# Optimization experiments

Hardware: AMD Instinct MI355X
Metric: run time of the kernel (lower is better)

Reference implementation:

```python
import jax, jax.numpy as jnp
import numpy as np

SAMPLERATE = 22050
N_OCTAVES = 16
N_SAMPLES = 32768
MIN_FREQ = 20.0 / (SAMPLERATE // 2)
MAX_FREQ = 3000.0 / (SAMPLERATE // 2)
FREQ_RANGE = MAX_FREQ - MIN_FREQ
BASE_RESONANCE = 0.01


def max_norm(x, axis=-1, eps=1e-8):
    return x / (jnp.max(jnp.abs(x), axis=axis, keepdims=True) + eps)


def exponential_decay(decay_values, n_octaves):
    # decay_values: (B, E, 1). Note the original applies sigmoid here on top of
    # the sigmoid already applied in forward (sigmoid_decay=True) -> double sigmoid.
    dv = jax.nn.sigmoid(decay_values)  # (B, E, 1)
    resonance_factor = (1.0 - BASE_RESONANCE) * 0.99
    decay = BASE_RESONANCE + dv * resonance_factor  # (B, E, 1)
    logd = jnp.log(decay + 1e-12)
    b, e, _ = decay_values.shape
    # cumsum of a per-(b,e) constant over octaves, then exp (matches torch code;
    # F.interpolate to size==n_octaves is the identity here)
    logd = jnp.broadcast_to(logd, (b, e, n_octaves))
    return jnp.exp(jnp.cumsum(logd, axis=-1))  # (B, E, O)


def setup_inputs() -> dict:
    key = jax.random.key(0)
    k1, k2, k3 = jax.random.split(key, 3)
    B, E = 8, 64
    return {
        "f0": jax.random.uniform(k1, (B, E, 1), dtype=jnp.float32),
        "decay_coefficients": jax.random.normal(k2, (B, E, 1), dtype=jnp.float32),
        "unused": jnp.zeros((B, E, 1), dtype=jnp.float32),
        "freq_spacing": jax.random.uniform(k3, (B, E, 1), dtype=jnp.float32),
    }


def reference(f0, decay_coefficients, unused, freq_spacing):
    b, e, _ = f0.shape
    O, S = N_OCTAVES, N_SAMPLES

    f0 = jnp.abs(f0)  # (B, E, 1)
    # sigmoid_decay=True path: sigmoid applied before exponential_decay
    exp_decays = exponential_decay(jax.nn.sigmoid(decay_coefficients), O)  # (B, E, O)

    f0 = (MIN_FREQ + f0 * FREQ_RANGE) * jnp.pi  # (B, E, 1)

    # freq_spacing repeated over octaves then cumsum -> per-octave factors
    factors = jnp.cumsum(jnp.broadcast_to(freq_spacing, (b, e, O)), axis=-1)
    f0s = f0 * factors  # (B, E, O)

    # nyquist cutoff
    f0s = f0s * (f0s < 1.0)

    # phase: cumsum over samples of constant per-octave frequency (faithful to torch)
    phase = jnp.cumsum(jnp.broadcast_to(f0s[..., None], (b, e, O, S)), axis=-1)
    osc = jnp.sin(phase)  # (B, E, O, S)

    osc = osc * exp_decays[..., None]
    osc = jnp.sum(osc, axis=2)  # (B, E, S)
    return max_norm(osc, axis=-1)
```

## Files before the change

### kernel.cpp

```cpp
#include <hip/hip_runtime.h>
#include <hip/hip_fp16.h>
#include <math.h>

#define N_OCT 16
#define NPAIR 8
#define NS    32768
#define TPB   512
#define SPT   (NS / TPB)
#define N_BE  512

typedef float v2f __attribute__((ext_vector_type(2)));
typedef _Float16 h4 __attribute__((ext_vector_type(4)));

static __device__ __forceinline__ v2f fma2(v2f a, v2f b, v2f c) {
    return __builtin_elementwise_fma(a, b, c);
}

#define WS_R(ws)    ((double*)(ws))
#define WS_C2H(ws)  ((float*)((char*)(ws) + 65536))
#define WS_C2L(ws)  ((float*)((char*)(ws) + 98304))
#define WS_AMP(ws)  ((float*)((char*)(ws) + 131072))

__global__ __launch_bounds__(256)
void f0res_setup(const float* __restrict__ f0_in,
                 const float* __restrict__ dc_in,
                 const float* __restrict__ fs_in,
                 void* __restrict__ ws)
{
    const int idx = blockIdx.x * 256 + threadIdx.x;
    if (idx >= N_BE * N_OCT) return;
    const int be = idx >> 4, o = idx & 15;

    const float f0a = fabsf(f0_in[be]);
    const float dc  = dc_in[be];
    const float fs  = fs_in[be];

    const float MINF = (float)(20.0 / 11025.0);
    const float FRNG = (float)(3000.0 / 11025.0 - 20.0 / 11025.0);

    const float s1    = 1.0f / (1.0f + __expf(-dc));
    const float dv    = 1.0f / (1.0f + __expf(-s1));
    const float decay = 0.01f + dv * 0.9801f;
    const float logd  = __logf(decay + 1e-12f);
    const float f0r   = (MINF + f0a * FRNG) * 3.14159274101257324f;

    float cl = 0.f, cf = 0.f;
    for (int i = 0; i <= o; ++i) { cl += logd; cf += fs; }
    float ed  = __expf(cl);
    float f0s = f0r * cf;
    float a   = ed;
    if (!(f0s < 1.0f)) { a = 0.0f; f0s = 0.0f; }

    const double inv2pi = 0.15915494309189535;
    double r = (double)f0s * inv2pi;

    double drev = r * (double)TPB;
    drev -= floor(drev);
    double c2d = 2.0 * cos(drev * 6.283185307179586);
    float  ch  = (float)c2d;

    WS_R(ws)[idx]   = r;
    WS_C2H(ws)[idx] = ch;
    WS_C2L(ws)[idx] = (float)(c2d - (double)ch);
    WS_AMP(ws)[idx] = a;
}

__global__ __launch_bounds__(TPB, 1)
void f0res_kernel(const void* __restrict__ ws,
                  float* __restrict__ out)
{
    extern __shared__ _Float16 smem[];
    __shared__ float wmax[TPB / 64];

    const int be = blockIdx.x;
    const int t  = threadIdx.x;

    const double* __restrict__ Rtab = WS_R(ws)   + be * N_OCT;
    const float*  __restrict__ CH   = WS_C2H(ws) + be * N_OCT;
    const float*  __restrict__ CLo  = WS_C2L(ws) + be * N_OCT;
    const float*  __restrict__ AMP  = WS_AMP(ws) + be * N_OCT;

    v2f xp[NPAIR], xc[NPAIR], c2h[NPAIR], c2l[NPAIR];

    #pragma unroll
    for (int o = 0; o < N_OCT; ++o) {
        const double r = Rtab[o];
        const float  a = AMP[o];

        double p0 = r * (double)(t + 1);
        p0 -= floor(p0);
        double pm = r * (double)(t + 1 - TPB);
        pm -= floor(pm);
        float xcur  = a * __builtin_amdgcn_sinf((float)p0);
        float xprev = a * __builtin_amdgcn_sinf((float)pm);

        const int j = o >> 1;
        if ((o & 1) == 0) {
            xc[j].x = xcur;   xp[j].x = xprev;
            c2h[j].x = CH[o]; c2l[j].x = CLo[o];
        } else {
            xc[j].y = xcur;   xp[j].y = xprev;
            c2h[j].y = CH[o]; c2l[j].y = CLo[o];
        }
    }

    float lmax = 0.0f;
    #pragma unroll 4
    for (int k = 0; k < SPT; ++k) {
        v2f acc2 = (v2f)(0.0f);
        #pragma unroll
        for (int j = 0; j < NPAIR; ++j) {
            acc2 += xc[j];
            v2f xn = fma2(c2h[j], xc[j], fma2(c2l[j], xc[j], -xp[j]));
            xp[j] = xc[j];
            xc[j] = xn;
        }
        float acc = acc2.x + acc2.y;
        smem[k * TPB + t] = (_Float16)acc;
        lmax = fmaxf(lmax, fabsf(acc));
    }

    #pragma unroll
    for (int off = 32; off > 0; off >>= 1)
        lmax = fmaxf(lmax, __shfl_down(lmax, off, 64));
    if ((t & 63) == 0) wmax[t >> 6] = lmax;
    __syncthreads();
    float bmax = wmax[0];
    #pragma unroll
    for (int w = 1; w < TPB / 64; ++w) bmax = fmaxf(bmax, wmax[w]);

    const float norm = 1.0f / (bmax + 1e-8f);
    float4* out4 = (float4*)(out + (size_t)be * NS);
    #pragma unroll
    for (int j = 0; j < NS / 4 / TPB; ++j) {
        int i = j * TPB + t;
        h4 v = *(const h4*)(smem + 4 * (size_t)i);
        float4 o;
        o.x = (float)v.x * norm; o.y = (float)v.y * norm;
        o.z = (float)v.z * norm; o.w = (float)v.w * norm;
        out4[i] = o;
    }
}

extern "C" void kernel_launch(void* const* d_in, const int* in_sizes, int n_in,
                              void* d_out, int out_size, void* d_ws, size_t ws_size,
                              hipStream_t stream) {
    const float* f0 = (const float*)d_in[0];
    const float* dc = (const float*)d_in[1];
    const float* fs = (const float*)d_in[3];
    float* out = (float*)d_out;

    hipLaunchKernelGGL(f0res_setup, dim3((N_BE * N_OCT + 255) / 256), dim3(256),
                       0, stream, f0, dc, fs, d_ws);
    hipLaunchKernelGGL(f0res_kernel, dim3(N_BE), dim3(TPB),
                       NS * sizeof(_Float16), stream, d_ws, out);
}
```

Before: 99.58 us.

## Fuse setup into main kernel and recompute oscillator instead of staging in LDS

Moves the per-octave parameter setup into the main kernel, computed by the first 16 threads into shared memory, which removes the separate setup launch and its workspace round trip. It also drops the fp16 LDS staging buffer. The recurrence now runs twice, once to find the max and once, with scaled initial state, to write normalized output directly. This trades twice the oscillator arithmetic for no 64KB LDS use and no fp16 rounding, and the output is now written with scalar strided stores instead of float4.

```diff
diff --git a/kernel.cpp b/kernel.cpp
--- a/kernel.cpp
+++ b/kernel.cpp
@@ -1,5 +1,4 @@
 #include <hip/hip_runtime.h>
-#include <hip/hip_fp16.h>
 #include <math.h>
 
 #define N_OCT 16
@@ -10,82 +9,67 @@
 #define N_BE  512
 
 typedef float v2f __attribute__((ext_vector_type(2)));
-typedef _Float16 h4 __attribute__((ext_vector_type(4)));
 
 static __device__ __forceinline__ v2f fma2(v2f a, v2f b, v2f c) {
     return __builtin_elementwise_fma(a, b, c);
 }
 
-#define WS_R(ws)    ((double*)(ws))
-#define WS_C2H(ws)  ((float*)((char*)(ws) + 65536))
-#define WS_C2L(ws)  ((float*)((char*)(ws) + 98304))
-#define WS_AMP(ws)  ((float*)((char*)(ws) + 131072))
-
-__global__ __launch_bounds__(256)
-void f0res_setup(const float* __restrict__ f0_in,
-                 const float* __restrict__ dc_in,
-                 const float* __restrict__ fs_in,
-                 void* __restrict__ ws)
-{
-    const int idx = blockIdx.x * 256 + threadIdx.x;
-    if (idx >= N_BE * N_OCT) return;
-    const int be = idx >> 4, o = idx & 15;
-
-    const float f0a = fabsf(f0_in[be]);
-    const float dc  = dc_in[be];
-    const float fs  = fs_in[be];
-
-    const float MINF = (float)(20.0 / 11025.0);
-    const float FRNG = (float)(3000.0 / 11025.0 - 20.0 / 11025.0);
-
-    const float s1    = 1.0f / (1.0f + __expf(-dc));
-    const float dv    = 1.0f / (1.0f + __expf(-s1));
-    const float decay = 0.01f + dv * 0.9801f;
-    const float logd  = __logf(decay + 1e-12f);
-    const float f0r   = (MINF + f0a * FRNG) * 3.14159274101257324f;
-
-    float cl = 0.f, cf = 0.f;
-    for (int i = 0; i <= o; ++i) { cl += logd; cf += fs; }
-    float ed  = __expf(cl);
-    float f0s = f0r * cf;
-    float a   = ed;
-    if (!(f0s < 1.0f)) { a = 0.0f; f0s = 0.0f; }
-
-    const double inv2pi = 0.15915494309189535;
-    double r = (double)f0s * inv2pi;
-
-    double drev = r * (double)TPB;
-    drev -= floor(drev);
-    double c2d = 2.0 * cos(drev * 6.283185307179586);
-    float  ch  = (float)c2d;
-
-    WS_R(ws)[idx]   = r;
-    WS_C2H(ws)[idx] = ch;
-    WS_C2L(ws)[idx] = (float)(c2d - (double)ch);
-    WS_AMP(ws)[idx] = a;
-}
-
 __global__ __launch_bounds__(TPB, 1)
-void f0res_kernel(const void* __restrict__ ws,
+void f0res_kernel(const float* __restrict__ f0_in,
+                  const float* __restrict__ dc_in,
+                  const float* __restrict__ fs_in,
                   float* __restrict__ out)
 {
-    extern __shared__ _Float16 smem[];
-    __shared__ float wmax[TPB / 64];
+    __shared__ double sR[N_OCT];
+    __shared__ float  sCH[N_OCT], sCL[N_OCT], sAMP[N_OCT];
+    __shared__ float  wmax[TPB / 64];
 
     const int be = blockIdx.x;
     const int t  = threadIdx.x;
 
-    const double* __restrict__ Rtab = WS_R(ws)   + be * N_OCT;
-    const float*  __restrict__ CH   = WS_C2H(ws) + be * N_OCT;
-    const float*  __restrict__ CLo  = WS_C2L(ws) + be * N_OCT;
-    const float*  __restrict__ AMP  = WS_AMP(ws) + be * N_OCT;
+    if (t < N_OCT) {
+        const int o = t;
+        const float f0a = fabsf(f0_in[be]);
+        const float dc  = dc_in[be];
+        const float fs  = fs_in[be];
 
-    v2f xp[NPAIR], xc[NPAIR], c2h[NPAIR], c2l[NPAIR];
+        const float MINF = (float)(20.0 / 11025.0);
+        const float FRNG = (float)(3000.0 / 11025.0 - 20.0 / 11025.0);
+
+        const float s1    = 1.0f / (1.0f + __expf(-dc));
+        const float dv    = 1.0f / (1.0f + __expf(-s1));
+        const float decay = 0.01f + dv * 0.9801f;
+        const float logd  = __logf(decay + 1e-12f);
+        const float f0r   = (MINF + f0a * FRNG) * 3.14159274101257324f;
+
+        float cl = 0.f, cf = 0.f;
+        for (int i = 0; i <= o; ++i) { cl += logd; cf += fs; }
+        float ed  = __expf(cl);
+        float f0s = f0r * cf;
+        float a   = ed;
+        if (!(f0s < 1.0f)) { a = 0.0f; f0s = 0.0f; }
+
+        const double inv2pi = 0.15915494309189535;
+        double r = (double)f0s * inv2pi;
+
+        double drev = r * (double)TPB;
+        drev -= floor(drev);
+        double c2d = 2.0 * cos(drev * 6.283185307179586);
+        float  ch  = (float)c2d;
+
+        sR[o]   = r;
+        sCH[o]  = ch;
+        sCL[o]  = (float)(c2d - (double)ch);
+        sAMP[o] = a;
+    }
+    __syncthreads();
+
+    v2f xp[NPAIR], xc[NPAIR], c2h[NPAIR], c2l[NPAIR], sx[NPAIR], sp[NPAIR];
 
     #pragma unroll
     for (int o = 0; o < N_OCT; ++o) {
-        const double r = Rtab[o];
-        const float  a = AMP[o];
+        const double r = sR[o];
+        const float  a = sAMP[o];
 
         double p0 = r * (double)(t + 1);
         p0 -= floor(p0);
@@ -97,12 +81,14 @@
         const int j = o >> 1;
         if ((o & 1) == 0) {
             xc[j].x = xcur;   xp[j].x = xprev;
-            c2h[j].x = CH[o]; c2l[j].x = CLo[o];
+            c2h[j].x = sCH[o]; c2l[j].x = sCL[o];
         } else {
             xc[j].y = xcur;   xp[j].y = xprev;
-            c2h[j].y = CH[o]; c2l[j].y = CLo[o];
+            c2h[j].y = sCH[o]; c2l[j].y = sCL[o];
         }
     }
+    #pragma unroll
+    for (int j = 0; j < NPAIR; ++j) { sx[j] = xc[j]; sp[j] = xp[j]; }
 
     float lmax = 0.0f;
     #pragma unroll 4
@@ -115,9 +101,7 @@
             xp[j] = xc[j];
             xc[j] = xn;
         }
-        float acc = acc2.x + acc2.y;
-        smem[k * TPB + t] = (_Float16)acc;
-        lmax = fmaxf(lmax, fabsf(acc));
+        lmax = fmaxf(lmax, fabsf(acc2.x + acc2.y));
     }
 
     #pragma unroll
@@ -130,15 +114,25 @@
     for (int w = 1; w < TPB / 64; ++w) bmax = fmaxf(bmax, wmax[w]);
 
     const float norm = 1.0f / (bmax + 1e-8f);
-    float4* out4 = (float4*)(out + (size_t)be * NS);
+
     #pragma unroll
-    for (int j = 0; j < NS / 4 / TPB; ++j) {
-        int i = j * TPB + t;
-        h4 v = *(const h4*)(smem + 4 * (size_t)i);
-        float4 o;
-        o.x = (float)v.x * norm; o.y = (float)v.y * norm;
-        o.z = (float)v.z * norm; o.w = (float)v.w * norm;
-        out4[i] = o;
+    for (int j = 0; j < NPAIR; ++j) {
+        xc[j] = sx[j] * norm;
+        xp[j] = sp[j] * norm;
+    }
+
+    float* __restrict__ orow = out + (size_t)be * NS;
+    #pragma unroll 4
+    for (int k = 0; k < SPT; ++k) {
+        v2f acc2 = (v2f)(0.0f);
+        #pragma unroll
+        for (int j = 0; j < NPAIR; ++j) {
+            acc2 += xc[j];
+            v2f xn = fma2(c2h[j], xc[j], fma2(c2l[j], xc[j], -xp[j]));
+            xp[j] = xc[j];
+            xc[j] = xn;
+        }
+        orow[k * TPB + t] = acc2.x + acc2.y;
     }
 }
 
@@ -149,9 +143,8 @@
     const float* dc = (const float*)d_in[1];
     const float* fs = (const float*)d_in[3];
     float* out = (float*)d_out;
+    (void)d_ws; (void)ws_size;
 
-    hipLaunchKernelGGL(f0res_setup, dim3((N_BE * N_OCT + 255) / 256), dim3(256),
-                       0, stream, f0, dc, fs, d_ws);
     hipLaunchKernelGGL(f0res_kernel, dim3(N_BE), dim3(TPB),
-                       NS * sizeof(_Float16), stream, d_ws, out);
+                       0, stream, f0, dc, fs, out);
 }
```

After: 109.4 us. 1.1x slower.
